# Kernel tuning notes

Hardware: AMD Instinct MI355X
Metric: run time of the kernel (lower is better)

Reference implementation:

```python
import jax, jax.numpy as jnp
import numpy as np

N_NODES = 50000
N_EDGES = 600000
IN_CH, HID, EMB = 128, 128, 64


def _glorot(key, shape):
    fan_in, fan_out = shape[1], shape[0]
    lim = np.sqrt(6.0 / (fan_in + fan_out))
    return jax.random.uniform(key, shape, jnp.float32, -lim, lim)


def setup_inputs() -> dict:
    key = jax.random.key(0)
    ks = jax.random.split(key, 12)
    x = jax.random.normal(ks[0], (N_NODES, IN_CH), jnp.float32)
    edge_index = jax.random.randint(ks[1], (2, N_EDGES), 0, N_NODES, jnp.int64)
    return {
        "x": x,
        "edge_index": edge_index,
        # SAGEConv layer 1: lin_l (neighbor, with bias) + lin_r (root, no bias)
        "w1n": _glorot(ks[2], (HID, IN_CH)),
        "w1r": _glorot(ks[3], (HID, IN_CH)),
        "b1": jnp.zeros((HID,), jnp.float32),
        "w2n": _glorot(ks[4], (HID, HID)),
        "w2r": _glorot(ks[5], (HID, HID)),
        "b2": jnp.zeros((HID,), jnp.float32),
        "w3n": _glorot(ks[6], (EMB, HID)),
        "w3r": _glorot(ks[7], (EMB, HID)),
        "b3": jnp.zeros((EMB,), jnp.float32),
    }


def _sage_conv(x, src, dst, wn, wr, b):
    # mean aggregation of source-node features at destination nodes
    msg = x[src]                                            # [E, d_in]
    agg = jax.ops.segment_sum(msg, dst, num_segments=N_NODES)
    deg = jax.ops.segment_sum(jnp.ones((src.shape[0],), x.dtype), dst,
                              num_segments=N_NODES)
    agg = agg / jnp.maximum(deg, 1.0)[:, None]
    return agg @ wn.T + x @ wr.T + b


def reference(x, edge_index, w1n, w1r, b1, w2n, w2r, b2, w3n, w3r, b3):
    src, dst = edge_index[0], edge_index[1]
    h = jax.nn.relu(_sage_conv(x, src, dst, w1n, w1r, b1))
    # dropout(p=0.3) is identity in inference mode
    h = jax.nn.relu(_sage_conv(h, src, dst, w2n, w2r, b2))
    h = _sage_conv(h, src, dst, w3n, w3r, b3)
    return h
```

## Files before the change

### kernel.cpp

```cpp
#include <hip/hip_runtime.h>
#include <hip/hip_bf16.h>

#define NN 50000
#define ZROW 50000
#define ELLW 64
#define F8MINDEG 6

#define NB 128
#define BSH 9
#define BCAP 8192
#define EPB 2048

typedef short bf16x8 __attribute__((ext_vector_type(8)));
typedef float f32x4 __attribute__((ext_vector_type(4)));
typedef float floatx2 __attribute__((ext_vector_type(2)));

#if __has_builtin(__builtin_amdgcn_cvt_pk_f32_fp8) && __has_builtin(__builtin_amdgcn_cvt_pk_fp8_f32)
#define HWF8 1
#endif

__device__ __forceinline__ float bf_lo(unsigned int p) {
    union { unsigned int u; float f; } c; c.u = p << 16; return c.f;
}
__device__ __forceinline__ float bf_hi(unsigned int p) {
    union { unsigned int u; float f; } c; c.u = p & 0xffff0000u; return c.f;
}
__device__ __forceinline__ unsigned short bfbits(float f) {
    __hip_bfloat16 h = __float2bfloat16(f);
    union { __hip_bfloat16 b; unsigned short s; } c; c.b = h; return c.s;
}
__device__ __forceinline__ unsigned int pack_bf(float a, float b) {
    return (unsigned int)bfbits(a) | ((unsigned int)bfbits(b) << 16);
}
__device__ __forceinline__ void stv(float* p, float v) { *p = v; }
__device__ __forceinline__ void stv(unsigned short* p, float v) { *p = bfbits(v); }

__device__ __forceinline__ floatx2 bfpair(unsigned int p) {
    union { unsigned int u; float f; } lo, hi;
    lo.u = p << 16; hi.u = p & 0xffff0000u;
    return floatx2{lo.f, hi.f};
}
__device__ __forceinline__ void acc8v(const uint4& u, floatx2* a) {
    a[0] += bfpair(u.x); a[1] += bfpair(u.y);
    a[2] += bfpair(u.z); a[3] += bfpair(u.w);
}

__device__ __forceinline__ unsigned int enc1(float f) {
#ifdef HWF8
    return (unsigned int)__builtin_amdgcn_cvt_pk_fp8_f32(f, f, 0, false) & 0xffu;
#else
    union { float f; unsigned u; } c; c.f = f;
    unsigned s = (c.u >> 24) & 0x80u;
    float af = fabsf(f);
    if (af >= 448.f) return s | 0x7eu;
    if (af < 0.0078125f) {
        unsigned m = (unsigned)(af * 512.f + 0.5f);
        return s | (m > 7u ? 7u : m);
    }
    unsigned u = c.u & 0x7fffffffu;
    u += 0x7ffffu + ((u >> 20) & 1u);
    int e = (int)(u >> 23) - 120;
    if (e < 1) { unsigned m = (unsigned)(af * 512.f + 0.5f); return s | (m > 7u ? 7u : m); }
    if (e > 15) return s | 0x7eu;
    return s | ((unsigned)e << 3) | ((u >> 20) & 7u);
#endif
}
__device__ __forceinline__ unsigned int packf8_4(float x, float y, float z, float w) {
#ifdef HWF8
    int u = __builtin_amdgcn_cvt_pk_fp8_f32(x, y, 0, false);
    u = __builtin_amdgcn_cvt_pk_fp8_f32(z, w, u, true);
    return (unsigned int)u;
#else
    return enc1(x) | (enc1(y) << 8) | (enc1(z) << 16) | (enc1(w) << 24);
#endif
}
__device__ __forceinline__ void accf8v(const uint4& u, floatx2* a) {
#ifdef HWF8
    a[0] += __builtin_amdgcn_cvt_pk_f32_fp8(u.x, false);
    a[1] += __builtin_amdgcn_cvt_pk_f32_fp8(u.x, true);
    a[2] += __builtin_amdgcn_cvt_pk_f32_fp8(u.y, false);
    a[3] += __builtin_amdgcn_cvt_pk_f32_fp8(u.y, true);
    a[4] += __builtin_amdgcn_cvt_pk_f32_fp8(u.z, false);
    a[5] += __builtin_amdgcn_cvt_pk_f32_fp8(u.z, true);
    a[6] += __builtin_amdgcn_cvt_pk_f32_fp8(u.w, false);
    a[7] += __builtin_amdgcn_cvt_pk_f32_fp8(u.w, true);
#else
    const unsigned ww[4] = {u.x, u.y, u.z, u.w};
#pragma unroll
    for (int k = 0; k < 4; k++) {
#pragma unroll
        for (int j = 0; j < 4; j++) {
            unsigned b = (ww[k] >> (8 * j)) & 0xffu;
            unsigned v = ((b & 0x80u) << 24) | (((b & 0x7fu) + (120u << 3)) << 20);
            if ((b & 0x78u) == 0) v = 0u;
            union { unsigned u; float f; } c; c.u = v;
            a[(k * 4 + j) >> 1][(k * 4 + j) & 1] += c.f;
        }
    }
#endif
}

__global__ __launch_bounds__(256) void wb3z_kernel(
    const float* __restrict__ w1n, const float* __restrict__ w1r,
    const float* __restrict__ w2n, const float* __restrict__ w2r,
    const float* __restrict__ w3n, const float* __restrict__ w3r,
    unsigned short* __restrict__ wB1, unsigned short* __restrict__ wB2,
    unsigned short* __restrict__ wB3, int* __restrict__ zblk,
    unsigned short* __restrict__ xb, unsigned short* __restrict__ axc,
    unsigned short* __restrict__ h1b,
    unsigned char* __restrict__ xf8, unsigned char* __restrict__ h1f8) {
    int i = blockIdx.x * blockDim.x + threadIdx.x;
    if (i < 2048) zblk[i] = 0;
    int p = i - 2048;
    if (p >= 0 && p < 256) {
        if (p < 64)       ((unsigned int*)(xb  + (size_t)ZROW * 128))[p] = 0u;
        else if (p < 128) ((unsigned int*)(axc + (size_t)ZROW * 128))[p - 64] = 0u;
        else if (p < 192) ((unsigned int*)(h1b + (size_t)ZROW * 128))[p - 128] = 0u;
        else if (p < 224) ((unsigned int*)(xf8 + (size_t)ZROW * 128))[p - 192] = 0u;
        else              ((unsigned int*)(h1f8 + (size_t)ZROW * 128))[p - 224] = 0u;
    }
    if (i >= 12288) return;
    if (i < 8192) {
        const float* wn = (i < 4096) ? w1n : w2n;
        const float* wr = (i < 4096) ? w1r : w2r;
        unsigned short* wB = (i < 4096) ? wB1 : wB2;
        int li = i & 4095;
        int row = li >> 5;
        int j = (li & 31) * 4;
        float4 a = *(const float4*)(wn + (size_t)row * 128 + j);
        float4 b = *(const float4*)(wr + (size_t)row * 128 + j);
        *(uint2*)(wB + (size_t)row * 256 + j) = uint2{pack_bf(a.x, a.y), pack_bf(a.z, a.w)};
        *(uint2*)(wB + (size_t)row * 256 + 128 + j) = uint2{pack_bf(b.x, b.y), pack_bf(b.z, b.w)};
    } else {
        int li = i - 8192;
        const float* w = (li < 2048) ? w3n : w3r;
        int rbase = (li < 2048) ? 0 : 64;
        int lj = li & 2047;
        int row = lj >> 5;
        int j = (lj & 31) * 4;
        float4 a = *(const float4*)(w + (size_t)row * 128 + j);
        *(uint2*)(wB3 + (size_t)(rbase + row) * 128 + j) =
            uint2{pack_bf(a.x, a.y), pack_bf(a.z, a.w)};
    }
}

__global__ __launch_bounds__(256) void binify_cvt_kernel(
    const float* __restrict__ x,
    unsigned short* __restrict__ xb,
    unsigned char* __restrict__ xf8,
    const int* __restrict__ src,
    const int* __restrict__ dst,
    unsigned int* __restrict__ bpos,
    unsigned int* __restrict__ barr,
    int n4, int E, int nEB) {
    __shared__ int cnt[NB];
    __shared__ int gbase[NB];
    const int t = threadIdx.x;
    const int blk = blockIdx.x;
    if (blk < nEB) {
        int e0 = blk * EPB;
        int ss[8], dd[8], rr[8];
        bool v[8];
#pragma unroll
        for (int k = 0; k < 8; k++) {
            int e = e0 + t + (k << 8);
            v[k] = (e < E);
            ss[k] = v[k] ? src[e] : 0;
            dd[k] = v[k] ? dst[e] : 0;
            rr[k] = 0;
        }
        if (t < NB) cnt[t] = 0;
        __syncthreads();
#pragma unroll
        for (int k = 0; k < 8; k++)
            if (v[k]) rr[k] = atomicAdd(&cnt[dd[k] >> BSH], 1);
        __syncthreads();
        if (t < NB) {
            int c = cnt[t];
            gbase[t] = c ? (int)atomicAdd(&bpos[t], (unsigned)c) : 0;
        }
        __syncthreads();
#pragma unroll
        for (int k = 0; k < 8; k++) {
            if (v[k]) {
                int b = dd[k] >> BSH;
                int pos = gbase[b] + rr[k];
                if (pos < BCAP)
                    barr[b * BCAP + pos] =
                        (unsigned)ss[k] | ((unsigned)dd[k] << 16);
            }
        }
    }
    int gtid = blk * 256 + t;
    int gs = gridDim.x << 8;
    for (int i = gtid; i < n4; i += gs) {
        float4 vv = *(const float4*)(x + 4 * (size_t)i);
        *(uint2*)(xb + 4 * (size_t)i) = uint2{pack_bf(vv.x, vv.y), pack_bf(vv.z, vv.w)};
        *(unsigned int*)(xf8 + 4 * (size_t)i) = packf8_4(vv.x, vv.y, vv.z, vv.w);
    }
}

__global__ __launch_bounds__(256) void ellbuild_kernel(
    const unsigned int* __restrict__ bpos,
    const unsigned int* __restrict__ barr,
    unsigned short* __restrict__ ell,
    int* __restrict__ cnt) {
    __shared__ alignas(16) unsigned short lell[512 * 64];
    __shared__ int lcnt[512];
    const int t = threadIdx.x;
    const int b = blockIdx.x;
    const unsigned PADP = 0xC350C350u;
    for (int i = t; i < 4096; i += 256) ((uint4*)lell)[i] = uint4{PADP, PADP, PADP, PADP};
    for (int i = t; i < 512; i += 256) lcnt[i] = 0;
    __syncthreads();
    int ne = (int)bpos[b];
    if (ne > BCAP) ne = BCAP;
    const unsigned int* seg = barr + (size_t)b * BCAP;
    for (int i = t; i < ne; i += 256) {
        unsigned p = seg[i];
        int ln = (p >> 16) & 511;
        int r = atomicAdd(&lcnt[ln], 1);
        lell[(ln << 6) + (r & (ELLW - 1))] = (unsigned short)(p & 0xffffu);
    }
    __syncthreads();
    int node0 = b << BSH;
    int nn = NN - node0;
    if (nn > 512) nn = 512;
    if (nn <= 0) return;
    uint4* gell = (uint4*)(ell + (size_t)node0 * ELLW);
    const uint4* sell = (const uint4*)lell;
    for (int i = t; i < nn * 8; i += 256) gell[i] = sell[i];
    for (int i = t; i < nn; i += 256) cnt[node0 + i] = lcnt[i];
}

__global__ __launch_bounds__(256) void gather_kernel(
    const int* __restrict__ cnt, const unsigned short* __restrict__ ell,
    const unsigned char* __restrict__ hf8,
    const unsigned short* __restrict__ hb,
    unsigned short* __restrict__ axc,
    int n_nodes) {
    int tid = blockIdx.x * blockDim.x + threadIdx.x;
    int n = tid >> 3;
    if (n >= n_nodes) return;
    int c = (tid & 7) << 4;
    int deg = cnt[n];
    int dd8 = (min(deg, ELLW) + 7) & ~7;
    const unsigned short* cl = ell + (size_t)n * ELLW;
    floatx2 a[8];
#pragma unroll
    for (int k = 0; k < 8; k++) a[k] = floatx2{0.f, 0.f};
    if (deg >= F8MINDEG) {
        for (int i = 0; i < dd8; i += 8) {
            uint4 idv = *(const uint4*)(cl + i);
            int i0 = idv.x & 0xffff, i1 = idv.x >> 16;
            int i2 = idv.y & 0xffff, i3 = idv.y >> 16;
            int i4 = idv.z & 0xffff, i5 = idv.z >> 16;
            int i6 = idv.w & 0xffff, i7 = idv.w >> 16;
            uint4 u0 = *(const uint4*)(hf8 + (size_t)i0 * 128 + c);
            uint4 u1 = *(const uint4*)(hf8 + (size_t)i1 * 128 + c);
            uint4 u2 = *(const uint4*)(hf8 + (size_t)i2 * 128 + c);
            uint4 u3 = *(const uint4*)(hf8 + (size_t)i3 * 128 + c);
            uint4 u4 = *(const uint4*)(hf8 + (size_t)i4 * 128 + c);
            uint4 u5 = *(const uint4*)(hf8 + (size_t)i5 * 128 + c);
            uint4 u6 = *(const uint4*)(hf8 + (size_t)i6 * 128 + c);
            uint4 u7 = *(const uint4*)(hf8 + (size_t)i7 * 128 + c);
            accf8v(u0, a); accf8v(u1, a); accf8v(u2, a); accf8v(u3, a);
            accf8v(u4, a); accf8v(u5, a); accf8v(u6, a); accf8v(u7, a);
        }
    } else {
        for (int i = 0; i < dd8; i += 8) {
            uint4 idv = *(const uint4*)(cl + i);
            int is[8];
            is[0] = idv.x & 0xffff; is[1] = idv.x >> 16;
            is[2] = idv.y & 0xffff; is[3] = idv.y >> 16;
            is[4] = idv.z & 0xffff; is[5] = idv.z >> 16;
            is[6] = idv.w & 0xffff; is[7] = idv.w >> 16;
#pragma unroll
            for (int k = 0; k < 8; k++) {
                uint4 lo = *(const uint4*)(hb + (size_t)is[k] * 128 + c);
                uint4 hi = *(const uint4*)(hb + (size_t)is[k] * 128 + c + 8);
                acc8v(lo, a); acc8v(hi, a + 4);
            }
        }
    }
    float s = 1.0f / (float)max(deg, 1);
    uint4 p0 = {pack_bf(a[0][0] * s, a[0][1] * s), pack_bf(a[1][0] * s, a[1][1] * s),
                pack_bf(a[2][0] * s, a[2][1] * s), pack_bf(a[3][0] * s, a[3][1] * s)};
    uint4 p1 = {pack_bf(a[4][0] * s, a[4][1] * s), pack_bf(a[5][0] * s, a[5][1] * s),
                pack_bf(a[6][0] * s, a[6][1] * s), pack_bf(a[7][0] * s, a[7][1] * s)};
    *(uint4*)(axc + (size_t)n * 128 + c) = p0;
    *(uint4*)(axc + (size_t)n * 128 + c + 8) = p1;
}

__global__ __launch_bounds__(256) void gather_add_kernel(
    const int* __restrict__ cnt, const unsigned short* __restrict__ ell,
    const unsigned short* __restrict__ tu,
    const float* __restrict__ b3,
    float* __restrict__ out, int n_nodes) {
    int tid = blockIdx.x * blockDim.x + threadIdx.x;
    int n = tid >> 3;
    if (n >= n_nodes) return;
    int c = (tid & 7) << 3;
    int deg = cnt[n];
    int dd8 = (min(deg, ELLW) + 7) & ~7;
    const unsigned short* cl = ell + (size_t)n * ELLW;
    floatx2 a[4];
#pragma unroll
    for (int k = 0; k < 4; k++) a[k] = floatx2{0.f, 0.f};
    for (int i = 0; i < dd8; i += 8) {
        uint4 idv = *(const uint4*)(cl + i);
        int i0 = idv.x & 0xffff, i1 = idv.x >> 16;
        int i2 = idv.y & 0xffff, i3 = idv.y >> 16;
        int i4 = idv.z & 0xffff, i5 = idv.z >> 16;
        int i6 = idv.w & 0xffff, i7 = idv.w >> 16;
        uint4 u0 = *(const uint4*)(tu + (size_t)i0 * 128 + c);
        uint4 u1 = *(const uint4*)(tu + (size_t)i1 * 128 + c);
        uint4 u2 = *(const uint4*)(tu + (size_t)i2 * 128 + c);
        uint4 u3 = *(const uint4*)(tu + (size_t)i3 * 128 + c);
        uint4 u4 = *(const uint4*)(tu + (size_t)i4 * 128 + c);
        uint4 u5 = *(const uint4*)(tu + (size_t)i5 * 128 + c);
        uint4 u6 = *(const uint4*)(tu + (size_t)i6 * 128 + c);
        uint4 u7 = *(const uint4*)(tu + (size_t)i7 * 128 + c);
        acc8v(u0, a); acc8v(u1, a); acc8v(u2, a); acc8v(u3, a);
        acc8v(u4, a); acc8v(u5, a); acc8v(u6, a); acc8v(u7, a);
    }
    float s = 1.0f / (float)max(deg, 1);
    uint4 uu = *(const uint4*)(tu + (size_t)n * 128 + 64 + c);
    float4 bA = *(const float4*)(b3 + c);
    float4 bB = *(const float4*)(b3 + c + 4);
    float* o = out + (size_t)n * 64 + c;
    o[0] = a[0][0] * s + bf_lo(uu.x) + bA.x;
    o[1] = a[0][1] * s + bf_hi(uu.x) + bA.y;
    o[2] = a[1][0] * s + bf_lo(uu.y) + bA.z;
    o[3] = a[1][1] * s + bf_hi(uu.y) + bA.w;
    o[4] = a[2][0] * s + bf_lo(uu.z) + bB.x;
    o[5] = a[2][1] * s + bf_hi(uu.z) + bB.y;
    o[6] = a[3][0] * s + bf_lo(uu.w) + bB.z;
    o[7] = a[3][1] * s + bf_hi(uu.w) + bB.w;
}

template <int NKS, bool RELU, bool BIAS, bool F8, typename OUT_T>
__global__ __launch_bounds__(256) void mfma_gemm(
    const unsigned short* __restrict__ A0, const unsigned short* __restrict__ A1,
    const unsigned short* __restrict__ B,
    const float* __restrict__ bias,
    OUT_T* __restrict__ out, unsigned char* __restrict__ f8out,
    int M) {
    constexpr int KTOT = NKS * 64;
    __shared__ unsigned short As[2][128 * 72];
    __shared__ unsigned short Bs[2][128 * 72];
    const int t = threadIdx.x;
    const int w = t >> 6, l = t & 63;
    const int m0 = blockIdx.x * 128;
    const int lr = l & 15, lq = l >> 4;

#pragma unroll
    for (int j = 0; j < 4; j++) {
        int c = t + j * 256;
        int row = c >> 3;
        int ko = (c & 7) * 8;
        int gm = m0 + row;
        uint4 va = {0u, 0u, 0u, 0u};
        if (gm < M) va = *(const uint4*)(A0 + (size_t)gm * 128 + ko);
        *(uint4*)(&As[0][row * 72 + ko]) = va;
        *(uint4*)(&Bs[0][row * 72 + ko]) = *(const uint4*)(B + (size_t)row * KTOT + ko);
    }
    __syncthreads();

    f32x4 acc[2][8];
#pragma unroll
    for (int tm = 0; tm < 2; tm++)
#pragma unroll
        for (int tn = 0; tn < 8; tn++) acc[tm][tn] = f32x4{0.f, 0.f, 0.f, 0.f};

#pragma unroll
    for (int ks = 0; ks < NKS; ks++) {
        uint4 pfA[4], pfB[4];
        if (ks + 1 < NKS) {
            int ns = ks + 1;
            const unsigned short* Asrc = (ns < NKS / 2)
                ? (A0 + (size_t)ns * 64) : (A1 + (size_t)(ns - NKS / 2) * 64);
#pragma unroll
            for (int j = 0; j < 4; j++) {
                int c = t + j * 256;
                int row = c >> 3;
                int ko = (c & 7) * 8;
                int gm = m0 + row;
                pfA[j] = uint4{0u, 0u, 0u, 0u};
                if (gm < M) pfA[j] = *(const uint4*)(Asrc + (size_t)gm * 128 + ko);
                pfB[j] = *(const uint4*)(B + (size_t)row * KTOT + ns * 64 + ko);
            }
        }
        const unsigned short* as = As[ks & 1];
        const unsigned short* bs = Bs[ks & 1];
#pragma unroll
        for (int kc = 0; kc < 2; kc++) {
            int lk = kc * 32 + lq * 8;
            bf16x8 af[2], bfr[8];
            af[0] = *(const bf16x8*)(&as[(w * 32 + lr) * 72 + lk]);
            af[1] = *(const bf16x8*)(&as[(w * 32 + 16 + lr) * 72 + lk]);
#pragma unroll
            for (int tn = 0; tn < 8; tn++)
                bfr[tn] = *(const bf16x8*)(&bs[(tn * 16 + lr) * 72 + lk]);
#pragma unroll
            for (int tm = 0; tm < 2; tm++)
#pragma unroll
                for (int tn = 0; tn < 8; tn++)
                    acc[tm][tn] = __builtin_amdgcn_mfma_f32_16x16x32_bf16(
                        af[tm], bfr[tn], acc[tm][tn], 0, 0, 0);
        }
        if (ks + 1 < NKS) {
#pragma unroll
            for (int j = 0; j < 4; j++) {
                int c = t + j * 256;
                int row = c >> 3;
                int ko = (c & 7) * 8;
                *(uint4*)(&As[(ks + 1) & 1][row * 72 + ko]) = pfA[j];
                *(uint4*)(&Bs[(ks + 1) & 1][row * 72 + ko]) = pfB[j];
            }
            __syncthreads();
        }
    }

#pragma unroll
    for (int tn = 0; tn < 8; tn++) {
        int n = tn * 16 + lr;
        float bj = BIAS ? bias[n] : 0.f;
#pragma unroll
        for (int tm = 0; tm < 2; tm++) {
#pragma unroll
            for (int i = 0; i < 4; i++) {
                int m = m0 + w * 32 + tm * 16 + lq * 4 + i;
                if (m < M) {
                    float v = acc[tm][tn][i] + bj;
                    if (RELU) v = fmaxf(v, 0.f);
                    stv(&out[(size_t)m * 128 + n], v);
                    if (F8) f8out[(size_t)m * 128 + n] = (unsigned char)enc1(v);
                }
            }
        }
    }
}

extern "C" void kernel_launch(void* const* d_in, const int* in_sizes, int n_in,
                              void* d_out, int out_size, void* d_ws, size_t ws_size,
                              hipStream_t stream) {
    const float* x  = (const float*)d_in[0];
    const int* ei   = (const int*)d_in[1];
    const float* w1n = (const float*)d_in[2];
    const float* w1r = (const float*)d_in[3];
    const float* b1  = (const float*)d_in[4];
    const float* w2n = (const float*)d_in[5];
    const float* w2r = (const float*)d_in[6];
    const float* b2  = (const float*)d_in[7];
    const float* w3n = (const float*)d_in[8];
    const float* w3r = (const float*)d_in[9];
    const float* b3  = (const float*)d_in[10];
    float* out = (float*)d_out;

    const int E = in_sizes[1] / 2;
    const int* src = ei;
    const int* dst = ei + E;

    char* ws = (char*)d_ws;
    unsigned short* xb  = (unsigned short*)(ws);
    unsigned short* axc = (unsigned short*)(ws + 13000000);
    unsigned short* h1b = (unsigned short*)(ws + 26000000);
    unsigned short* h2b = (unsigned short*)(ws + 39000000);
    unsigned int* barr  = (unsigned int*)(ws + 39000000);
    unsigned short* ell = (unsigned short*)(ws + 52000000);
    int* cnt            = (int*)  (ws + 64800000);
    int* zblk           = (int*)  (ws + 65400000);
    unsigned int* bpos  = (unsigned int*)(zblk + 1536);
    unsigned short* wB1 = (unsigned short*)(ws + 65500000);
    unsigned short* wB2 = (unsigned short*)(ws + 65600000);
    unsigned short* wB3 = (unsigned short*)(ws + 65700000);
    unsigned char* xf8  = (unsigned char*)(ws + 65800000);
    unsigned char* h1f8 = (unsigned char*)(ws + 72300000);

    const int nEB = (E + EPB - 1) / EPB;

    wb3z_kernel<<<48, 256, 0, stream>>>(
        w1n, w1r, w2n, w2r, w3n, w3r, wB1, wB2, wB3, zblk, xb, axc, h1b, xf8, h1f8);
    binify_cvt_kernel<<<2048, 256, 0, stream>>>(x, xb, xf8, src, dst,
                                                bpos, barr, NN * 32, E, nEB);
    ellbuild_kernel<<<(NN + 511) / 512, 256, 0, stream>>>(bpos, barr, ell, cnt);

    const int gatherBlocks = (NN * 8 + 255) / 256;
    const int mTiles = (NN + 127) / 128;

    gather_kernel<<<gatherBlocks, 256, 0, stream>>>(cnt, ell, xf8, xb, axc, NN);
    mfma_gemm<4, true, true, true, unsigned short>
        <<<mTiles, 256, 0, stream>>>(axc, xb, wB1, b1, h1b, h1f8, NN);

    gather_kernel<<<gatherBlocks, 256, 0, stream>>>(cnt, ell, h1f8, h1b, axc, NN);
    mfma_gemm<4, true, true, false, unsigned short>
        <<<mTiles, 256, 0, stream>>>(axc, h1b, wB2, b2, h2b, nullptr, NN);

    mfma_gemm<2, false, false, false, unsigned short>
        <<<mTiles, 256, 0, stream>>>(h2b, h2b + 64, wB3, nullptr, axc, nullptr, NN);
    gather_add_kernel<<<gatherBlocks, 256, 0, stream>>>(
        cnt, ell, axc, b3, out, NN);
}
```

Measured before the change: 221.0 us.

## Fuse neighbor gather into layer GEMM via shared-memory aggregated tile

Replaces the separate gather and GEMM kernels for layers 1 and 2 with one 512-thread kernel. It aggregates 128 node rows into shared memory, then runs MFMA against both that tile and the root features, which are read directly from global memory. This removes the write and re-read of the aggregated bf16 buffer and two kernel launches. In exchange, the gather now runs at 391-block granularity with larger blocks and heavy shared-memory use, which may lower occupancy and latency hiding for the random gather.

```diff
diff --git a/kernel.cpp b/kernel.cpp
--- a/kernel.cpp
+++ b/kernel.cpp
@@ -233,63 +233,147 @@
     for (int i = t; i < nn; i += 256) cnt[node0 + i] = lcnt[i];
 }
 
-__global__ __launch_bounds__(256) void gather_kernel(
+template <bool F8>
+__global__ __launch_bounds__(512) void fused_layer(
     const int* __restrict__ cnt, const unsigned short* __restrict__ ell,
     const unsigned char* __restrict__ hf8,
     const unsigned short* __restrict__ hb,
-    unsigned short* __restrict__ axc,
-    int n_nodes) {
-    int tid = blockIdx.x * blockDim.x + threadIdx.x;
-    int n = tid >> 3;
-    if (n >= n_nodes) return;
-    int c = (tid & 7) << 4;
-    int deg = cnt[n];
-    int dd8 = (min(deg, ELLW) + 7) & ~7;
-    const unsigned short* cl = ell + (size_t)n * ELLW;
-    floatx2 a[8];
-#pragma unroll
-    for (int k = 0; k < 8; k++) a[k] = floatx2{0.f, 0.f};
-    if (deg >= F8MINDEG) {
-        for (int i = 0; i < dd8; i += 8) {
-            uint4 idv = *(const uint4*)(cl + i);
-            int i0 = idv.x & 0xffff, i1 = idv.x >> 16;
-            int i2 = idv.y & 0xffff, i3 = idv.y >> 16;
-            int i4 = idv.z & 0xffff, i5 = idv.z >> 16;
-            int i6 = idv.w & 0xffff, i7 = idv.w >> 16;
-            uint4 u0 = *(const uint4*)(hf8 + (size_t)i0 * 128 + c);
-            uint4 u1 = *(const uint4*)(hf8 + (size_t)i1 * 128 + c);
-            uint4 u2 = *(const uint4*)(hf8 + (size_t)i2 * 128 + c);
-            uint4 u3 = *(const uint4*)(hf8 + (size_t)i3 * 128 + c);
-            uint4 u4 = *(const uint4*)(hf8 + (size_t)i4 * 128 + c);
-            uint4 u5 = *(const uint4*)(hf8 + (size_t)i5 * 128 + c);
-            uint4 u6 = *(const uint4*)(hf8 + (size_t)i6 * 128 + c);
-            uint4 u7 = *(const uint4*)(hf8 + (size_t)i7 * 128 + c);
-            accf8v(u0, a); accf8v(u1, a); accf8v(u2, a); accf8v(u3, a);
-            accf8v(u4, a); accf8v(u5, a); accf8v(u6, a); accf8v(u7, a);
-        }
-    } else {
-        for (int i = 0; i < dd8; i += 8) {
-            uint4 idv = *(const uint4*)(cl + i);
-            int is[8];
-            is[0] = idv.x & 0xffff; is[1] = idv.x >> 16;
-            is[2] = idv.y & 0xffff; is[3] = idv.y >> 16;
-            is[4] = idv.z & 0xffff; is[5] = idv.z >> 16;
-            is[6] = idv.w & 0xffff; is[7] = idv.w >> 16;
-#pragma unroll
-            for (int k = 0; k < 8; k++) {
-                uint4 lo = *(const uint4*)(hb + (size_t)is[k] * 128 + c);
-                uint4 hi = *(const uint4*)(hb + (size_t)is[k] * 128 + c + 8);
-                acc8v(lo, a); acc8v(hi, a + 4);
-            }
-        }
-    }
-    float s = 1.0f / (float)max(deg, 1);
-    uint4 p0 = {pack_bf(a[0][0] * s, a[0][1] * s), pack_bf(a[1][0] * s, a[1][1] * s),
-                pack_bf(a[2][0] * s, a[2][1] * s), pack_bf(a[3][0] * s, a[3][1] * s)};
-    uint4 p1 = {pack_bf(a[4][0] * s, a[4][1] * s), pack_bf(a[5][0] * s, a[5][1] * s),
-                pack_bf(a[6][0] * s, a[6][1] * s), pack_bf(a[7][0] * s, a[7][1] * s)};
-    *(uint4*)(axc + (size_t)n * 128 + c) = p0;
-    *(uint4*)(axc + (size_t)n * 128 + c + 8) = p1;
+    const unsigned short* __restrict__ B,
+    const float* __restrict__ bias,
+    unsigned short* __restrict__ outb,
+    unsigned char* __restrict__ outf8,
+    int M) {
+    __shared__ unsigned short AsG[2][128 * 72];
+    __shared__ unsigned short Bs[2][128 * 72];
+    const int t = threadIdx.x;
+    const int w = t >> 6, l = t & 63;
+    const int lr = l & 15, lq = l >> 4;
+    const int m0 = blockIdx.x * 128;
+
+#pragma unroll
+    for (int j = 0; j < 2; j++) {
+        int c = t + j * 512;
+        int row = c >> 3;
+        int ko = (c & 7) * 8;
+        *(uint4*)(&Bs[0][row * 72 + ko]) = *(const uint4*)(B + (size_t)row * 256 + ko);
+    }
+
+#pragma unroll
+    for (int p = 0; p < 2; p++) {
+        int r = p * 64 + (t >> 3);
+        int n = m0 + r;
+        int ch = (t & 7) << 4;
+        int deg = (n < NN) ? cnt[n] : 0;
+        int dd8 = (min(deg, ELLW) + 7) & ~7;
+        const unsigned short* cl = ell + (size_t)n * ELLW;
+        floatx2 a[8];
+#pragma unroll
+        for (int k = 0; k < 8; k++) a[k] = floatx2{0.f, 0.f};
+        if (deg >= F8MINDEG) {
+            for (int i = 0; i < dd8; i += 8) {
+                uint4 idv = *(const uint4*)(cl + i);
+                int i0 = idv.x & 0xffff, i1 = idv.x >> 16;
+                int i2 = idv.y & 0xffff, i3 = idv.y >> 16;
+                int i4 = idv.z & 0xffff, i5 = idv.z >> 16;
+                int i6 = idv.w & 0xffff, i7 = idv.w >> 16;
+                uint4 u0 = *(const uint4*)(hf8 + (size_t)i0 * 128 + ch);
+                uint4 u1 = *(const uint4*)(hf8 + (size_t)i1 * 128 + ch);
+                uint4 u2 = *(const uint4*)(hf8 + (size_t)i2 * 128 + ch);
+                uint4 u3 = *(const uint4*)(hf8 + (size_t)i3 * 128 + ch);
+                uint4 u4 = *(const uint4*)(hf8 + (size_t)i4 * 128 + ch);
+                uint4 u5 = *(const uint4*)(hf8 + (size_t)i5 * 128 + ch);
+                uint4 u6 = *(const uint4*)(hf8 + (size_t)i6 * 128 + ch);
+                uint4 u7 = *(const uint4*)(hf8 + (size_t)i7 * 128 + ch);
+                accf8v(u0, a); accf8v(u1, a); accf8v(u2, a); accf8v(u3, a);
+                accf8v(u4, a); accf8v(u5, a); accf8v(u6, a); accf8v(u7, a);
+            }
+        } else if (deg > 0) {
+            for (int i = 0; i < dd8; i += 8) {
+                uint4 idv = *(const uint4*)(cl + i);
+                int is[8];
+                is[0] = idv.x & 0xffff; is[1] = idv.x >> 16;
+                is[2] = idv.y & 0xffff; is[3] = idv.y >> 16;
+                is[4] = idv.z & 0xffff; is[5] = idv.z >> 16;
+                is[6] = idv.w & 0xffff; is[7] = idv.w >> 16;
+#pragma unroll
+                for (int k = 0; k < 8; k++) {
+                    uint4 lo = *(const uint4*)(hb + (size_t)is[k] * 128 + ch);
+                    uint4 hi = *(const uint4*)(hb + (size_t)is[k] * 128 + ch + 8);
+                    acc8v(lo, a); acc8v(hi, a + 4);
+                }
+            }
+        }
+        float s = 1.0f / (float)max(deg, 1);
+        uint4 p0 = {pack_bf(a[0][0] * s, a[0][1] * s), pack_bf(a[1][0] * s, a[1][1] * s),
+                    pack_bf(a[2][0] * s, a[2][1] * s), pack_bf(a[3][0] * s, a[3][1] * s)};
+        uint4 p1 = {pack_bf(a[4][0] * s, a[4][1] * s), pack_bf(a[5][0] * s, a[5][1] * s),
+                    pack_bf(a[6][0] * s, a[6][1] * s), pack_bf(a[7][0] * s, a[7][1] * s)};
+        int slab = (t & 7) >> 2;
+        int ck = ((t & 7) & 3) << 4;
+        *(uint4*)(&AsG[slab][r * 72 + ck]) = p0;
+        *(uint4*)(&AsG[slab][r * 72 + ck + 8]) = p1;
+    }
+    __syncthreads();
+
+    f32x4 acc[8];
+#pragma unroll
+    for (int tn = 0; tn < 8; tn++) acc[tn] = f32x4{0.f, 0.f, 0.f, 0.f};
+    const int arow = w * 16 + lr;
+    const size_t groot = (size_t)min(m0 + arow, ZROW) * 128;
+
+#pragma unroll
+    for (int ks = 0; ks < 4; ks++) {
+        uint4 pfB[2];
+        if (ks < 3) {
+#pragma unroll
+            for (int j = 0; j < 2; j++) {
+                int c = t + j * 512;
+                int row = c >> 3;
+                int ko = (c & 7) * 8;
+                pfB[j] = *(const uint4*)(B + (size_t)row * 256 + (ks + 1) * 64 + ko);
+            }
+        }
+        const unsigned short* bs = Bs[ks & 1];
+#pragma unroll
+        for (int kc = 0; kc < 2; kc++) {
+            int lk = kc * 32 + lq * 8;
+            bf16x8 af, bfr[8];
+            if (ks < 2) af = *(const bf16x8*)(&AsG[ks][arow * 72 + lk]);
+            else        af = *(const bf16x8*)(hb + groot + (ks - 2) * 64 + lk);
+#pragma unroll
+            for (int tn = 0; tn < 8; tn++)
+                bfr[tn] = *(const bf16x8*)(&bs[(tn * 16 + lr) * 72 + lk]);
+#pragma unroll
+            for (int tn = 0; tn < 8; tn++)
+                acc[tn] = __builtin_amdgcn_mfma_f32_16x16x32_bf16(
+                    af, bfr[tn], acc[tn], 0, 0, 0);
+        }
+        if (ks < 3) {
+#pragma unroll
+            for (int j = 0; j < 2; j++) {
+                int c = t + j * 512;
+                int row = c >> 3;
+                int ko = (c & 7) * 8;
+                *(uint4*)(&Bs[(ks + 1) & 1][row * 72 + ko]) = pfB[j];
+            }
+            __syncthreads();
+        }
+    }
+
+#pragma unroll
+    for (int tn = 0; tn < 8; tn++) {
+        int n = tn * 16 + lr;
+        float bj = bias[n];
+#pragma unroll
+        for (int i = 0; i < 4; i++) {
+            int m = m0 + w * 16 + lq * 4 + i;
+            if (m < M) {
+                float v = fmaxf(acc[tn][i] + bj, 0.f);
+                stv(&outb[(size_t)m * 128 + n], v);
+                if (F8) outf8[(size_t)m * 128 + n] = (unsigned char)enc1(v);
+            }
+        }
+    }
 }
 
 __global__ __launch_bounds__(256) void gather_add_kernel(
@@ -339,12 +423,12 @@
     o[7] = a[3][1] * s + bf_hi(uu.w) + bB.w;
 }
 
-template <int NKS, bool RELU, bool BIAS, bool F8, typename OUT_T>
+template <int NKS, bool RELU, bool BIAS, typename OUT_T>
 __global__ __launch_bounds__(256) void mfma_gemm(
     const unsigned short* __restrict__ A0, const unsigned short* __restrict__ A1,
     const unsigned short* __restrict__ B,
     const float* __restrict__ bias,
-    OUT_T* __restrict__ out, unsigned char* __restrict__ f8out,
+    OUT_T* __restrict__ out,
     int M) {
     constexpr int KTOT = NKS * 64;
     __shared__ unsigned short As[2][128 * 72];
@@ -435,7 +519,6 @@
                     float v = acc[tm][tn][i] + bj;
                     if (RELU) v = fmaxf(v, 0.f);
                     stv(&out[(size_t)m * 128 + n], v);
-                    if (F8) f8out[(size_t)m * 128 + n] = (unsigned char)enc1(v);
                 }
             }
         }
@@ -486,19 +569,16 @@
                                                 bpos, barr, NN * 32, E, nEB);
     ellbuild_kernel<<<(NN + 511) / 512, 256, 0, stream>>>(bpos, barr, ell, cnt);
 
-    const int gatherBlocks = (NN * 8 + 255) / 256;
     const int mTiles = (NN + 127) / 128;
 
-    gather_kernel<<<gatherBlocks, 256, 0, stream>>>(cnt, ell, xf8, xb, axc, NN);
-    mfma_gemm<4, true, true, true, unsigned short>
-        <<<mTiles, 256, 0, stream>>>(axc, xb, wB1, b1, h1b, h1f8, NN);
-
-    gather_kernel<<<gatherBlocks, 256, 0, stream>>>(cnt, ell, h1f8, h1b, axc, NN);
-    mfma_gemm<4, true, true, false, unsigned short>
-        <<<mTiles, 256, 0, stream>>>(axc, h1b, wB2, b2, h2b, nullptr, NN);
-
-    mfma_gemm<2, false, false, false, unsigned short>
-        <<<mTiles, 256, 0, stream>>>(h2b, h2b + 64, wB3, nullptr, axc, nullptr, NN);
-    gather_add_kernel<<<gatherBlocks, 256, 0, stream>>>(
+    fused_layer<true><<<mTiles, 512, 0, stream>>>(
+        cnt, ell, xf8, xb, wB1, b1, h1b, h1f8, NN);
+
+    fused_layer<false><<<mTiles, 512, 0, stream>>>(
+        cnt, ell, h1f8, h1b, wB2, b2, h2b, nullptr, NN);
+
+    mfma_gemm<2, false, false, unsigned short>
+        <<<mTiles, 256, 0, stream>>>(h2b, h2b + 64, wB3, nullptr, axc, NN);
+    gather_add_kernel<<<(NN * 8 + 255) / 256, 256, 0, stream>>>(
         cnt, ell, axc, b3, out, NN);
 }
```

Measured after the change: 201.7 us. -8.8%, faster.
